# Kernel optimization log

Hardware: AMD Instinct MI355X
Metric: run time of the kernel (lower is better)

The kernel has to match this reference:

```python
import jax, jax.numpy as jnp
import numpy as np

# column-index constants for the node feature matrix and edge attributes
VM, VA, PG, QG, PD, QD = 0, 1, 2, 3, 4, 5
G_COL, B_COL = 0, 1

N_NODES = 100000
N_EDGES = 3200000
N_FEAT = 6


def setup_inputs() -> dict:
    key = jax.random.key(0)
    k1, k2, k3, k4, k5, k6 = jax.random.split(key, 6)
    pred = jax.random.normal(k1, (N_NODES, N_FEAT), dtype=jnp.float32)
    target = jax.random.normal(k2, (N_NODES, N_FEAT), dtype=jnp.float32)
    src = jax.random.randint(k3, (N_EDGES,), 0, N_NODES, dtype=jnp.int32)
    dst = jax.random.randint(k4, (N_EDGES,), 0, N_NODES, dtype=jnp.int32)
    edge_index = jnp.stack([src, dst], axis=0)
    edge_attr = jax.random.normal(k5, (N_EDGES, 2), dtype=jnp.float32)
    mask = jax.random.bernoulli(k6, 0.5, (N_NODES, N_FEAT))
    return {"pred": pred, "target": target, "edge_index": edge_index,
            "edge_attr": edge_attr, "mask": mask}


def reference(pred, target, edge_index, edge_attr, mask):
    # temp_pred[~mask] = target[~mask]
    tp = jnp.where(mask, pred, target)

    V_m = tp[:, VM]
    V_a = tp[:, VA]
    V = V_m * jnp.exp(1j * V_a)           # complex64 [N]
    V_conj = jnp.conj(V)

    # conj(Y_bus) entries on edges: G - jB
    Y_conj = edge_attr[:, G_COL] - 1j * edge_attr[:, B_COL]  # complex64 [E]

    row, col = edge_index[0], edge_index[1]
    # (Y_bus_conj @ V_conj)[i] = sum over edges (i,j) of conj(Y_ij) * conj(V_j)
    msg = Y_conj * V_conj[col]                               # gather-multiply [E]
    matvec = jax.ops.segment_sum(msg, row, num_segments=tp.shape[0])  # scatter-add [N]

    S_injection = V * matvec                                  # diag(V) @ (...)

    net_P = tp[:, PG] - tp[:, PD]
    net_Q = tp[:, QG] - tp[:, QD]
    diff = (net_P + 1j * net_Q) - S_injection

    loss = jnp.mean(jnp.abs(diff))
    real_loss = jnp.mean(jnp.abs(jnp.real(diff)))
    imag_loss = jnp.mean(jnp.abs(jnp.imag(diff)))
    return (loss, real_loss, imag_loss)
```

## Files before the change

### kernel.cpp

```cpp
#include <hip/hip_runtime.h>
#include <hip/hip_fp16.h>
#include <math.h>

constexpr int N_NODES = 100000;
constexpr int N_EDGES = 3200000;
constexpr int NF      = 6;

constexpr int BSHIFT  = 10;
constexpr int BNODES  = 1 << BSHIFT;
constexpr int NB      = (N_NODES + BNODES - 1) >> BSHIFT;
constexpr int CAP     = 33792;
constexpr int NSLICE  = 16;
constexpr int TILE    = 2048;
constexpr int EPT     = TILE / 256;
constexpr int NBLK_PART = (N_EDGES + TILE - 1) / TILE;
constexpr int VPREP_BLOCKS = (N_NODES + 255) / 256;
constexpr int NBLK_FIN  = (N_NODES + 255) / 256;

constexpr size_t OFF_V    = 0;
constexpr size_t OFF_REC  = OFF_V  + (size_t)N_NODES * 8;
constexpr size_t OFF_PART = OFF_REC + (size_t)NB * CAP * 8;
constexpr size_t OFF_CNT  = OFF_PART + (size_t)NB * NSLICE * BNODES * 8;
constexpr size_t WS_NEED  = OFF_CNT + 1024;

__device__ __forceinline__ float2 half2u_to_f2(unsigned u) {
    __half2 h;
    *reinterpret_cast<unsigned*>(&h) = u;
    return __half22float2(h);
}

__global__ __launch_bounds__(256) void partition_edges(
        const int* __restrict__ row, const int* __restrict__ col,
        const float2* __restrict__ attr,
        const float* __restrict__ pred, const float* __restrict__ target,
        const unsigned char* __restrict__ mask,
        float2* __restrict__ v_out,
        unsigned int* __restrict__ gcur,
        uint2* __restrict__ rec_g) {
    __shared__ unsigned int hc[4][NB];
    __shared__ int dbase[NB];
    __shared__ unsigned int tot_s[NB];
    __shared__ uint2 rec_s[TILE];
    __shared__ unsigned char bkt_s[TILE];
    __shared__ int total_s;

    const int tid = threadIdx.x;
    const int w = tid >> 6;
    const int e0 = blockIdx.x * TILE;
    const int e_base = e0 + tid * EPT;
    const bool ok = e_base < N_EDGES;

    if (blockIdx.x < VPREP_BLOCKS) {
        int i = blockIdx.x * 256 + tid;
        if (i < N_NODES) {
            const int bb = i * NF;
            float vm = mask[bb + 0] ? pred[bb + 0] : target[bb + 0];
            float va = mask[bb + 1] ? pred[bb + 1] : target[bb + 1];
            float sn, cs;
            sincosf(va, &sn, &cs);
            v_out[i] = make_float2(vm * cs, vm * sn);
        }
    }

    for (int i = tid; i < 4 * NB; i += 256)
        (&hc[0][0])[i] = 0u;
    __syncthreads();

    int r[EPT];
    if (ok) {
        int4 ra = *(const int4*)(row + e_base);
        int4 rb = *(const int4*)(row + e_base + 4);
        r[0]=ra.x; r[1]=ra.y; r[2]=ra.z; r[3]=ra.w;
        r[4]=rb.x; r[5]=rb.y; r[6]=rb.z; r[7]=rb.w;
        #pragma unroll
        for (int k = 0; k < EPT; ++k)
            atomicAdd(&hc[w][r[k] >> BSHIFT], 1u);
    }
    __syncthreads();

    if (tid < NB)
        tot_s[tid] = hc[0][tid] + hc[1][tid] + hc[2][tid] + hc[3][tid];
    __syncthreads();

    if (tid < NB) {
        int lbase = 0;
        for (int j = 0; j < tid; ++j) lbase += (int)tot_s[j];
        unsigned t0 = hc[0][tid], t1 = hc[1][tid], t2 = hc[2][tid];
        unsigned tot = tot_s[tid];
        unsigned g = tot ? atomicAdd(&gcur[tid], tot) : 0u;
        dbase[tid] = (int)g - lbase;
        hc[0][tid] = (unsigned)lbase;
        hc[1][tid] = (unsigned)(lbase + (int)t0);
        hc[2][tid] = (unsigned)(lbase + (int)(t0 + t1));
        hc[3][tid] = (unsigned)(lbase + (int)(t0 + t1 + t2));
        if (tid == NB - 1) total_s = lbase + (int)tot;
    }
    __syncthreads();

    if (ok) {
        int4 ca = *(const int4*)(col + e_base);
        int4 cb = *(const int4*)(col + e_base + 4);
        int c[EPT] = {ca.x, ca.y, ca.z, ca.w, cb.x, cb.y, cb.z, cb.w};
        float4 a0 = *(const float4*)(attr + e_base);
        float4 a1 = *(const float4*)(attr + e_base + 2);
        float4 a2 = *(const float4*)(attr + e_base + 4);
        float4 a3 = *(const float4*)(attr + e_base + 6);
        float gx[EPT] = {a0.x, a0.z, a1.x, a1.z, a2.x, a2.z, a3.x, a3.z};
        float gy[EPT] = {a0.y, a0.w, a1.y, a1.w, a2.y, a2.w, a3.y, a3.w};
        #pragma unroll
        for (int k = 0; k < EPT; ++k) {
            int rr = r[k];
            int b = rr >> BSHIFT;
            int slot = (int)atomicAdd(&hc[w][b], 1u);
            __half2 hh = __floats2half2_rn(gx[k], gy[k]);
            rec_s[slot] = make_uint2(
                (unsigned)c[k] | ((unsigned)(rr & (BNODES - 1)) << 17),
                *reinterpret_cast<unsigned int*>(&hh));
            bkt_s[slot] = (unsigned char)b;
        }
    }
    __syncthreads();

    const int total = total_s;
    for (int j = tid; j < total; j += 256) {
        int b = (int)bkt_s[j];
        int g = dbase[b] + j;
        if (g < CAP)
            rec_g[(size_t)b * CAP + g] = rec_s[j];
    }
}

__global__ __launch_bounds__(256) void accum_partials(
        const unsigned int* __restrict__ gcur,
        const uint2* __restrict__ rec,
        const float2* __restrict__ v,
        float2* __restrict__ partials) {
    __shared__ float acc_re[BNODES];
    __shared__ float acc_im[BNODES];
    const int tid = threadIdx.x;
    const int b = blockIdx.x / NSLICE;
    const int s = blockIdx.x % NSLICE;
    int cnt = (int)min(gcur[b], (unsigned)CAP);
    for (int i = tid; i < BNODES; i += 256) { acc_re[i] = 0.f; acc_im[i] = 0.f; }
    __syncthreads();
    int per = (((cnt + NSLICE - 1) / NSLICE) + 3) & ~3;
    int st = s * per;
    int en = min(st + per, cnt);
    const uint2* rp = rec + (size_t)b * CAP;
    int j = st + 4 * tid;
    for (; j + 3 < en; j += 1024) {
        uint4 q0 = *(const uint4*)(rp + j);
        uint4 q1 = *(const uint4*)(rp + j + 2);
        int c0 = (int)(q0.x & 0x1FFFFu), li0 = (int)(q0.x >> 17);
        int c1 = (int)(q0.z & 0x1FFFFu), li1 = (int)(q0.z >> 17);
        int c2 = (int)(q1.x & 0x1FFFFu), li2 = (int)(q1.x >> 17);
        int c3 = (int)(q1.z & 0x1FFFFu), li3 = (int)(q1.z >> 17);
        float2 vv0 = v[c0];
        float2 vv1 = v[c1];
        float2 vv2 = v[c2];
        float2 vv3 = v[c3];
        float2 gb0 = half2u_to_f2(q0.y);
        float2 gb1 = half2u_to_f2(q0.w);
        float2 gb2 = half2u_to_f2(q1.y);
        float2 gb3 = half2u_to_f2(q1.w);
        atomicAdd(&acc_re[li0], fmaf(gb0.x, vv0.x, -gb0.y * vv0.y));
        atomicAdd(&acc_im[li0], -fmaf(gb0.x, vv0.y, gb0.y * vv0.x));
        atomicAdd(&acc_re[li1], fmaf(gb1.x, vv1.x, -gb1.y * vv1.y));
        atomicAdd(&acc_im[li1], -fmaf(gb1.x, vv1.y, gb1.y * vv1.x));
        atomicAdd(&acc_re[li2], fmaf(gb2.x, vv2.x, -gb2.y * vv2.y));
        atomicAdd(&acc_im[li2], -fmaf(gb2.x, vv2.y, gb2.y * vv2.x));
        atomicAdd(&acc_re[li3], fmaf(gb3.x, vv3.x, -gb3.y * vv3.y));
        atomicAdd(&acc_im[li3], -fmaf(gb3.x, vv3.y, gb3.y * vv3.x));
    }
    for (; j < en; ++j) {
        uint2 q = rp[j];
        int c0 = (int)(q.x & 0x1FFFFu), li0 = (int)(q.x >> 17);
        float2 vv0 = v[c0];
        float2 gb0 = half2u_to_f2(q.y);
        atomicAdd(&acc_re[li0], fmaf(gb0.x, vv0.x, -gb0.y * vv0.y));
        atomicAdd(&acc_im[li0], -fmaf(gb0.x, vv0.y, gb0.y * vv0.x));
    }
    __syncthreads();
    float2* p = partials + ((size_t)b * NSLICE + s) * BNODES;
    for (int i = 2 * tid; i < BNODES; i += 512) {
        float4 q = make_float4(acc_re[i], acc_im[i], acc_re[i + 1], acc_im[i + 1]);
        *(float4*)(p + i) = q;
    }
}

__global__ __launch_bounds__(256) void finalize_nodes(
        const float2* __restrict__ partials,
        const float* __restrict__ pred,
        const float* __restrict__ target,
        const unsigned char* __restrict__ mask,
        const float2* __restrict__ v,
        float* __restrict__ sums,
        unsigned int* __restrict__ done_all,
        float* __restrict__ out) {
    const int tid = threadIdx.x;
    int i = blockIdx.x * 256 + tid;
    float a = 0.f, ar = 0.f, ai = 0.f;
    if (i < N_NODES) {
        const int b = i >> BSHIFT;
        const int li = i & (BNODES - 1);
        const float2* pb = partials + (size_t)b * NSLICE * BNODES + li;
        float mr = 0.f, mi = 0.f;
        #pragma unroll
        for (int s = 0; s < NSLICE; ++s) {
            float2 pp = pb[(size_t)s * BNODES];
            mr += pp.x; mi += pp.y;
        }
        const int bb = i * NF;
        float pg = mask[bb + 2] ? pred[bb + 2] : target[bb + 2];
        float qg = mask[bb + 3] ? pred[bb + 3] : target[bb + 3];
        float pd = mask[bb + 4] ? pred[bb + 4] : target[bb + 4];
        float qd = mask[bb + 5] ? pred[bb + 5] : target[bb + 5];
        float netP = pg - pd;
        float netQ = qg - qd;
        float2 vv = v[i];
        float s_re = vv.x * mr - vv.y * mi;
        float s_im = vv.x * mi + vv.y * mr;
        float dre = netP - s_re;
        float dim = netQ - s_im;
        ar = fabsf(dre);
        ai = fabsf(dim);
        a  = sqrtf(dre * dre + dim * dim);
    }
    #pragma unroll
    for (int off = 32; off > 0; off >>= 1) {
        a  += __shfl_down(a,  off, 64);
        ar += __shfl_down(ar, off, 64);
        ai += __shfl_down(ai, off, 64);
    }
    __shared__ float red[3][4];
    int wave = tid >> 6;
    int lane = tid & 63;
    if (lane == 0) { red[0][wave] = a; red[1][wave] = ar; red[2][wave] = ai; }
    __syncthreads();
    if (tid == 0) {
        float r0 = atomicAdd(&sums[0], red[0][0] + red[0][1] + red[0][2] + red[0][3]);
        float r1 = atomicAdd(&sums[1], red[1][0] + red[1][1] + red[1][2] + red[1][3]);
        float r2 = atomicAdd(&sums[2], red[2][0] + red[2][1] + red[2][2] + red[2][3]);
        float chk = r0 + r1 + r2;
        if (chk == chk) {
            unsigned fin = atomicAdd(done_all, 1u);
            if (fin == (unsigned)(NBLK_FIN - 1)) {
                const float inv = 1.0f / (float)N_NODES;
                float t0 = atomicAdd(&sums[0], 0.f);
                float t1 = atomicAdd(&sums[1], 0.f);
                float t2 = atomicAdd(&sums[2], 0.f);
                __hip_atomic_store(&out[0], t0 * inv, __ATOMIC_RELAXED, __HIP_MEMORY_SCOPE_AGENT);
                __hip_atomic_store(&out[1], t1 * inv, __ATOMIC_RELAXED, __HIP_MEMORY_SCOPE_AGENT);
                __hip_atomic_store(&out[2], t2 * inv, __ATOMIC_RELAXED, __HIP_MEMORY_SCOPE_AGENT);
            }
        }
    }
}

__global__ void node_prep_fb(const float* __restrict__ pred,
                             const float* __restrict__ target,
                             const unsigned char* __restrict__ mask,
                             float2* __restrict__ v) {
    int i = blockIdx.x * blockDim.x + threadIdx.x;
    if (i >= N_NODES) return;
    const int b = i * NF;
    float vm = mask[b + 0] ? pred[b + 0] : target[b + 0];
    float va = mask[b + 1] ? pred[b + 1] : target[b + 1];
    float s, c;
    sincosf(va, &s, &c);
    v[i] = make_float2(vm * c, vm * s);
}

__global__ void edge_scatter_fb(const int* __restrict__ row,
                                const int* __restrict__ col,
                                const float2* __restrict__ attr,
                                const float2* __restrict__ v,
                                float2* __restrict__ mv) {
    int e = blockIdx.x * blockDim.x + threadIdx.x;
    if (e >= N_EDGES) return;
    int r = row[e];
    int c = col[e];
    float2 gb = attr[e];
    float2 vv = v[c];
    float mre = fmaf(gb.x, vv.x, -gb.y * vv.y);
    float mim = -fmaf(gb.x, vv.y, gb.y * vv.x);
    atomicAdd(&mv[r].x, mre);
    atomicAdd(&mv[r].y, mim);
}

__global__ void finalize_fb(const float* __restrict__ pred,
                            const float* __restrict__ target,
                            const unsigned char* __restrict__ mask,
                            const float2* __restrict__ v,
                            const float2* __restrict__ mv,
                            float* __restrict__ sums) {
    int i = blockIdx.x * blockDim.x + threadIdx.x;
    float a = 0.f, ar = 0.f, ai = 0.f;
    if (i < N_NODES) {
        const int b = i * NF;
        float pg = mask[b + 2] ? pred[b + 2] : target[b + 2];
        float qg = mask[b + 3] ? pred[b + 3] : target[b + 3];
        float pd = mask[b + 4] ? pred[b + 4] : target[b + 4];
        float qd = mask[b + 5] ? pred[b + 5] : target[b + 5];
        float netP = pg - pd;
        float netQ = qg - qd;
        float2 vv = v[i];
        float2 m = mv[i];
        float s_re = vv.x * m.x - vv.y * m.y;
        float s_im = vv.x * m.y + vv.y * m.x;
        float dre = netP - s_re;
        float dim = netQ - s_im;
        ar = fabsf(dre);
        ai = fabsf(dim);
        a  = sqrtf(dre * dre + dim * dim);
    }
    #pragma unroll
    for (int off = 32; off > 0; off >>= 1) {
        a  += __shfl_down(a,  off, 64);
        ar += __shfl_down(ar, off, 64);
        ai += __shfl_down(ai, off, 64);
    }
    __shared__ float red[3][4];
    int wave = threadIdx.x >> 6;
    int lane = threadIdx.x & 63;
    if (lane == 0) { red[0][wave] = a; red[1][wave] = ar; red[2][wave] = ai; }
    __syncthreads();
    if (threadIdx.x == 0) {
        atomicAdd(&sums[0], red[0][0] + red[0][1] + red[0][2] + red[0][3]);
        atomicAdd(&sums[1], red[1][0] + red[1][1] + red[1][2] + red[1][3]);
        atomicAdd(&sums[2], red[2][0] + red[2][1] + red[2][2] + red[2][3]);
    }
}

__global__ void write_out_fb(const float* __restrict__ sums, float* __restrict__ out) {
    if (threadIdx.x == 0 && blockIdx.x == 0) {
        const float inv = 1.0f / (float)N_NODES;
        out[0] = sums[0] * inv;
        out[1] = sums[1] * inv;
        out[2] = sums[2] * inv;
    }
}

extern "C" void kernel_launch(void* const* d_in, const int* in_sizes, int n_in,
                              void* d_out, int out_size, void* d_ws, size_t ws_size,
                              hipStream_t stream) {
    const float*         pred   = (const float*)d_in[0];
    const float*         target = (const float*)d_in[1];
    const int*           eidx   = (const int*)d_in[2];
    const float2*        attr   = (const float2*)d_in[3];
    const unsigned char* mask   = (const unsigned char*)d_in[4];
    float* out = (float*)d_out;

    const int* row = eidx;
    const int* col = eidx + N_EDGES;

    char* ws = (char*)d_ws;
    const int B = 256;

    if (ws_size >= WS_NEED) {
        float2*       v        = (float2*)(ws + OFF_V);
        uint2*        rec_g    = (uint2*)(ws + OFF_REC);
        float2*       partials = (float2*)(ws + OFF_PART);
        unsigned int* gcur     = (unsigned int*)(ws + OFF_CNT);
        float*        sums     = (float*)(ws + OFF_CNT + 912);
        unsigned int* done_all = (unsigned int*)(ws + OFF_CNT + 928);

        hipMemsetAsync(ws + OFF_CNT, 0, 1024, stream);
        partition_edges<<<NBLK_PART, B, 0, stream>>>(row, col, attr,
                                                     pred, target, mask, v,
                                                     gcur, rec_g);
        accum_partials<<<NB * NSLICE, B, 0, stream>>>(gcur, rec_g, v, partials);
        finalize_nodes<<<NBLK_FIN, B, 0, stream>>>(partials, pred, target, mask, v,
                                                   sums, done_all, out);
    } else {
        float2* v    = (float2*)ws;
        float2* mv   = (float2*)(ws + (size_t)N_NODES * 8);
        float*  sums = (float*)(ws + 2ull * N_NODES * 8);
        hipMemsetAsync(mv, 0, (size_t)N_NODES * 8 + 16, stream);
        node_prep_fb<<<(N_NODES + B - 1) / B, B, 0, stream>>>(pred, target, mask, v);
        edge_scatter_fb<<<(N_EDGES + B - 1) / B, B, 0, stream>>>(row, col, attr, v, mv);
        finalize_fb<<<(N_NODES + B - 1) / B, B, 0, stream>>>(pred, target, mask, v, mv, sums);
        write_out_fb<<<1, 64, 0, stream>>>(sums, out);
    }
}
```

Before: 197.4 us.

## Fuse per-bucket accumulation with node finalize, halving bucket size

Buckets shrink from 1024 to 512 nodes, so there are twice as many of them. The per-bucket slicing into 16 partial blocks is removed. One block now accumulates all edges of its bucket in shared memory and computes the node residuals and loss sums directly. This drops the partials buffer write and read-back and one kernel launch. The cost is a much smaller grid of about 196 blocks, each walking roughly 16K edges serially, which may leave the GPU underoccupied for the latency-bound gathers.

```diff
diff --git a/kernel.cpp b/kernel.cpp
--- a/kernel.cpp
+++ b/kernel.cpp
@@ -6,21 +6,18 @@
 constexpr int N_EDGES = 3200000;
 constexpr int NF      = 6;
 
-constexpr int BSHIFT  = 10;
+constexpr int BSHIFT  = 9;
 constexpr int BNODES  = 1 << BSHIFT;
 constexpr int NB      = (N_NODES + BNODES - 1) >> BSHIFT;
-constexpr int CAP     = 33792;
-constexpr int NSLICE  = 16;
+constexpr int CAP     = 17408;
 constexpr int TILE    = 2048;
 constexpr int EPT     = TILE / 256;
 constexpr int NBLK_PART = (N_EDGES + TILE - 1) / TILE;
 constexpr int VPREP_BLOCKS = (N_NODES + 255) / 256;
-constexpr int NBLK_FIN  = (N_NODES + 255) / 256;
 
 constexpr size_t OFF_V    = 0;
 constexpr size_t OFF_REC  = OFF_V  + (size_t)N_NODES * 8;
-constexpr size_t OFF_PART = OFF_REC + (size_t)NB * CAP * 8;
-constexpr size_t OFF_CNT  = OFF_PART + (size_t)NB * NSLICE * BNODES * 8;
+constexpr size_t OFF_CNT  = OFF_REC + (size_t)NB * CAP * 8;
 constexpr size_t WS_NEED  = OFF_CNT + 1024;
 
 __device__ __forceinline__ float2 half2u_to_f2(unsigned u) {
@@ -130,25 +127,26 @@
     }
 }
 
-__global__ __launch_bounds__(256) void accum_partials(
+__global__ __launch_bounds__(256) void accum_finalize(
         const unsigned int* __restrict__ gcur,
         const uint2* __restrict__ rec,
+        const float* __restrict__ pred,
+        const float* __restrict__ target,
+        const unsigned char* __restrict__ mask,
         const float2* __restrict__ v,
-        float2* __restrict__ partials) {
+        float* __restrict__ sums,
+        unsigned int* __restrict__ done_all,
+        float* __restrict__ out) {
     __shared__ float acc_re[BNODES];
     __shared__ float acc_im[BNODES];
     const int tid = threadIdx.x;
-    const int b = blockIdx.x / NSLICE;
-    const int s = blockIdx.x % NSLICE;
+    const int b = blockIdx.x;
     int cnt = (int)min(gcur[b], (unsigned)CAP);
     for (int i = tid; i < BNODES; i += 256) { acc_re[i] = 0.f; acc_im[i] = 0.f; }
     __syncthreads();
-    int per = (((cnt + NSLICE - 1) / NSLICE) + 3) & ~3;
-    int st = s * per;
-    int en = min(st + per, cnt);
     const uint2* rp = rec + (size_t)b * CAP;
-    int j = st + 4 * tid;
-    for (; j + 3 < en; j += 1024) {
+    int j = 4 * tid;
+    for (; j + 3 < cnt; j += 1024) {
         uint4 q0 = *(const uint4*)(rp + j);
         uint4 q1 = *(const uint4*)(rp + j + 2);
         int c0 = (int)(q0.x & 0x1FFFFu), li0 = (int)(q0.x >> 17);
@@ -172,7 +170,7 @@
         atomicAdd(&acc_re[li3], fmaf(gb3.x, vv3.x, -gb3.y * vv3.y));
         atomicAdd(&acc_im[li3], -fmaf(gb3.x, vv3.y, gb3.y * vv3.x));
     }
-    for (; j < en; ++j) {
+    for (; j < cnt; ++j) {
         uint2 q = rp[j];
         int c0 = (int)(q.x & 0x1FFFFu), li0 = (int)(q.x >> 17);
         float2 vv0 = v[c0];
@@ -181,35 +179,13 @@
         atomicAdd(&acc_im[li0], -fmaf(gb0.x, vv0.y, gb0.y * vv0.x));
     }
     __syncthreads();
-    float2* p = partials + ((size_t)b * NSLICE + s) * BNODES;
-    for (int i = 2 * tid; i < BNODES; i += 512) {
-        float4 q = make_float4(acc_re[i], acc_im[i], acc_re[i + 1], acc_im[i + 1]);
-        *(float4*)(p + i) = q;
-    }
-}
-
-__global__ __launch_bounds__(256) void finalize_nodes(
-        const float2* __restrict__ partials,
-        const float* __restrict__ pred,
-        const float* __restrict__ target,
-        const unsigned char* __restrict__ mask,
-        const float2* __restrict__ v,
-        float* __restrict__ sums,
-        unsigned int* __restrict__ done_all,
-        float* __restrict__ out) {
-    const int tid = threadIdx.x;
-    int i = blockIdx.x * 256 + tid;
+
     float a = 0.f, ar = 0.f, ai = 0.f;
-    if (i < N_NODES) {
-        const int b = i >> BSHIFT;
-        const int li = i & (BNODES - 1);
-        const float2* pb = partials + (size_t)b * NSLICE * BNODES + li;
-        float mr = 0.f, mi = 0.f;
-        #pragma unroll
-        for (int s = 0; s < NSLICE; ++s) {
-            float2 pp = pb[(size_t)s * BNODES];
-            mr += pp.x; mi += pp.y;
-        }
+    for (int li = tid; li < BNODES; li += 256) {
+        int i = (b << BSHIFT) + li;
+        if (i >= N_NODES) break;
+        float mr = acc_re[li];
+        float mi = acc_im[li];
         const int bb = i * NF;
         float pg = mask[bb + 2] ? pred[bb + 2] : target[bb + 2];
         float qg = mask[bb + 3] ? pred[bb + 3] : target[bb + 3];
@@ -222,9 +198,9 @@
         float s_im = vv.x * mi + vv.y * mr;
         float dre = netP - s_re;
         float dim = netQ - s_im;
-        ar = fabsf(dre);
-        ai = fabsf(dim);
-        a  = sqrtf(dre * dre + dim * dim);
+        ar += fabsf(dre);
+        ai += fabsf(dim);
+        a  += sqrtf(dre * dre + dim * dim);
     }
     #pragma unroll
     for (int off = 32; off > 0; off >>= 1) {
@@ -244,7 +220,7 @@
         float chk = r0 + r1 + r2;
         if (chk == chk) {
             unsigned fin = atomicAdd(done_all, 1u);
-            if (fin == (unsigned)(NBLK_FIN - 1)) {
+            if (fin == (unsigned)(NB - 1)) {
                 const float inv = 1.0f / (float)N_NODES;
                 float t0 = atomicAdd(&sums[0], 0.f);
                 float t1 = atomicAdd(&sums[1], 0.f);
@@ -360,7 +336,6 @@
     if (ws_size >= WS_NEED) {
         float2*       v        = (float2*)(ws + OFF_V);
         uint2*        rec_g    = (uint2*)(ws + OFF_REC);
-        float2*       partials = (float2*)(ws + OFF_PART);
         unsigned int* gcur     = (unsigned int*)(ws + OFF_CNT);
         float*        sums     = (float*)(ws + OFF_CNT + 912);
         unsigned int* done_all = (unsigned int*)(ws + OFF_CNT + 928);
@@ -369,9 +344,9 @@
         partition_edges<<<NBLK_PART, B, 0, stream>>>(row, col, attr,
                                                      pred, target, mask, v,
                                                      gcur, rec_g);
-        accum_partials<<<NB * NSLICE, B, 0, stream>>>(gcur, rec_g, v, partials);
-        finalize_nodes<<<NBLK_FIN, B, 0, stream>>>(partials, pred, target, mask, v,
-                                                   sums, done_all, out);
+        accum_finalize<<<NB, B, 0, stream>>>(gcur, rec_g,
+                                             pred, target, mask, v,
+                                             sums, done_all, out);
     } else {
         float2* v    = (float2*)ws;
         float2* mv   = (float2*)(ws + (size_t)N_NODES * 8);
```

Result: no change. 195.1 us (-1.2%).
